# Performance work log

Measured on AMD Instinct MI355X. Metric: run time of the kernel, lower is better.

Reference implementation:

```python
import jax, jax.numpy as jnp
import numpy as np

NEG_BIG = -9e15

def setup_inputs() -> dict:
    key = jax.random.key(0)
    k1, k2, k3, k4 = jax.random.split(key, 4)
    N, Fin, Fout = 8192, 256, 128
    x = jax.random.normal(k1, (N, Fin), dtype=jnp.float32)
    adj = jax.random.randint(k2, (N, N), 0, 2, dtype=jnp.int32)
    # xavier-uniform-like init
    limW = float(np.sqrt(6.0 / (Fin + Fout)))
    W = jax.random.uniform(k3, (Fin, Fout), minval=-limW, maxval=limW, dtype=jnp.float32)
    lima = float(np.sqrt(6.0 / (2 * Fout + 1)))
    a = jax.random.uniform(k4, (2 * Fout, 1), minval=-lima, maxval=lima, dtype=jnp.float32)
    return {"x": x, "adj": adj, "W": W, "a": a}

def reference(x, adj, W, a, alpha=0.2):
    # h: (N, Fout)
    h = x @ W
    Fout = W.shape[1]
    # Split a into source/target halves: e[i,j] = leakyrelu(h_i·a1 + h_j·a2)
    a1, a2 = a[:Fout, 0], a[Fout:, 0]
    s = h @ a1  # (N,) row (source) scores
    t = h @ a2  # (N,) col (target) scores
    e = jax.nn.leaky_relu(s[:, None] + t[None, :], negative_slope=alpha)  # (N, N)
    e = jnp.where(adj > 0, e, NEG_BIG)
    attention = jax.nn.softmax(e, axis=1)
    # dropout omitted (eval mode / training=False)
    return attention @ h
```

## Files before the change

kernel.cpp:

```cpp
#include <hip/hip_runtime.h>
#include <hip/hip_bf16.h>

typedef __attribute__((ext_vector_type(8))) short short8;
typedef __attribute__((ext_vector_type(4))) short short4v;
typedef __attribute__((ext_vector_type(4))) float f32x4;

#define NR 8192
#define LOG2E 1.4426950408889634f

__device__ __forceinline__ short f2bf(float f) {
  return __builtin_bit_cast(short, __float2bfloat16(f));
}

__global__ __launch_bounds__(256) void k_gemm_h(const float* __restrict__ x,
                                                const float* __restrict__ W,
                                                const float* __restrict__ a,
                                                short* __restrict__ HT2,
                                                float* __restrict__ sv,
                                                float* __restrict__ tv) {
  __shared__ short WT[128][136];
  const int tid = threadIdx.x;
  const int w = tid >> 6;
  const int L = tid & 63;
  const int lm = L & 15;
  const int q = L >> 4;
  const int i0 = blockIdx.x * 64;

  f32x4 acc[8];
#pragma unroll
  for (int nn = 0; nn < 8; ++nn) acc[nn] = (f32x4){0.f, 0.f, 0.f, 0.f};

  for (int kc = 0; kc < 256; kc += 128) {
    if (kc) __syncthreads();
#pragma unroll
    for (int p = 0; p < 16; ++p) {
      int idx = p * 256 + tid;
      int k = idx >> 5;
      int f4 = (idx & 31) * 4;
      float4 v = *(const float4*)&W[(kc + k) * 128 + f4];
      WT[f4 + 0][k] = f2bf(v.x);
      WT[f4 + 1][k] = f2bf(v.y);
      WT[f4 + 2][k] = f2bf(v.z);
      WT[f4 + 3][k] = f2bf(v.w);
    }
    __syncthreads();
#pragma unroll
    for (int ks = 0; ks < 4; ++ks) {
      int row = i0 + 16 * w + lm;
      const float* xp = &x[(size_t)row * 256 + kc + ks * 32 + q * 8];
      float4 xa = *(const float4*)xp;
      float4 xb = *(const float4*)(xp + 4);
      short8 af;
      af[0] = f2bf(xa.x); af[1] = f2bf(xa.y); af[2] = f2bf(xa.z); af[3] = f2bf(xa.w);
      af[4] = f2bf(xb.x); af[5] = f2bf(xb.y); af[6] = f2bf(xb.z); af[7] = f2bf(xb.w);
#pragma unroll
      for (int nn = 0; nn < 8; ++nn) {
        short8 bf = *(const short8*)&WT[nn * 16 + lm][ks * 32 + q * 8];
        acc[nn] = __builtin_amdgcn_mfma_f32_16x16x32_bf16(af, bf, acc[nn], 0, 0, 0);
      }
    }
  }

  const int ib = i0 + 16 * w + 4 * q;
  const int tbase = (ib >> 5) * 4096 + (ib & 31);
  float a1v[8], a2v[8];
#pragma unroll
  for (int nn = 0; nn < 8; ++nn) {
    a1v[nn] = a[nn * 16 + lm];
    a2v[nn] = a[128 + nn * 16 + lm];
  }
  float sr[4] = {0.f, 0.f, 0.f, 0.f};
  float tr[4] = {0.f, 0.f, 0.f, 0.f};
#pragma unroll
  for (int nn = 0; nn < 8; ++nn) {
    int f = nn * 16 + lm;
    short4v o;
    o[0] = f2bf(acc[nn][0]);
    o[1] = f2bf(acc[nn][1]);
    o[2] = f2bf(acc[nn][2]);
    o[3] = f2bf(acc[nn][3]);
    *(short4v*)&HT2[tbase + f * 32] = o;
#pragma unroll
    for (int r = 0; r < 4; ++r) {
      sr[r] += acc[nn][r] * a1v[nn];
      tr[r] += acc[nn][r] * a2v[nn];
    }
  }
#pragma unroll
  for (int d = 1; d < 16; d <<= 1) {
#pragma unroll
    for (int r = 0; r < 4; ++r) {
      sr[r] += __shfl_xor(sr[r], d);
      tr[r] += __shfl_xor(tr[r], d);
    }
  }
  if (lm == 0) {
#pragma unroll
    for (int r = 0; r < 4; ++r) {
      sv[ib + r] = sr[r] * LOG2E;
      tv[ib + r] = tr[r] * LOG2E;
    }
  }
}

__global__ __launch_bounds__(256, 2) void k_flash(const int* __restrict__ adj,
                                                  const short* __restrict__ HT2,
                                                  const float* __restrict__ sv,
                                                  const float* __restrict__ tv,
                                                  float* __restrict__ part,
                                                  float* __restrict__ lpart) {
  __shared__ short lds_s[32768];
  unsigned* ldsw = (unsigned*)lds_s;
  const int tid = threadIdx.x;
  const int w = tid >> 6;
  const int L = tid & 63;
  const int lm = L & 15;
  const int q = L >> 4;
  const int sp = blockIdx.x & 15;
  const int it = blockIdx.x >> 4;
  const int i0 = it * 128;

  const int row0 = i0 + 32 * w + lm;
  const int row1 = row0 + 16;
  const float s0 = sv[row0];
  const float s1 = sv[row1];
  const size_t ar0 = (size_t)row0 * NR;
  const size_t ar1 = (size_t)row1 * NR;

  f32x4 acc[2][8];
#pragma unroll
  for (int mm = 0; mm < 2; ++mm)
#pragma unroll
    for (int nn = 0; nn < 8; ++nn) acc[mm][nn] = (f32x4){0.f, 0.f, 0.f, 0.f};
  float l0 = 0.f, l1 = 0.f;

  const int tile0 = sp * 16;
  int jb = tile0 * 32 + q * 8;
  int4 sa00 = *(const int4*)&adj[ar0 + jb];
  int4 sa01 = *(const int4*)&adj[ar0 + jb + 4];
  int4 sa10 = *(const int4*)&adj[ar1 + jb];
  int4 sa11 = *(const int4*)&adj[ar1 + jb + 4];

  for (int t = 0; t < 16; ++t) {
    if ((t & 7) == 0) {
      __syncthreads();
      const int pbase_t = tile0 + t;
#pragma unroll
      for (int z = 0; z < 16; ++z) {
        int id = z * 256 + tid;
        int tt = id >> 9;
        int k = id & 511;
        int f = k >> 2, c = k & 3;
        uint4 v = *(const uint4*)&HT2[(size_t)(pbase_t + tt) * 4096 + k * 8];
        int cs = c ^ ((f >> 1) & 3);
        *(uint4*)&ldsw[tt * 2048 + f * 16 + cs * 4] = v;
      }
      __syncthreads();
    }
    int4 a00 = sa00, a01 = sa01, a10 = sa10, a11 = sa11;
    if (t + 1 < 16) {
      int jn = (tile0 + t + 1) * 32 + q * 8;
      sa00 = *(const int4*)&adj[ar0 + jn];
      sa01 = *(const int4*)&adj[ar0 + jn + 4];
      sa10 = *(const int4*)&adj[ar1 + jn];
      sa11 = *(const int4*)&adj[ar1 + jn + 4];
    }
    const int jc = (tile0 + t) * 32 + q * 8;
    float4 tv0 = *(const float4*)&tv[jc];
    float4 tv1 = *(const float4*)&tv[jc + 4];
    const int tt = t & 7;
    short8 bf[8];
#pragma unroll
    for (int nn = 0; nn < 8; ++nn) {
      int f = nn * 16 + lm;
      bf[nn] = *(const short8*)&ldsw[tt * 2048 + f * 16 + ((q ^ ((f >> 1) & 3)) * 4)];
    }

    int av0[8] = {a00.x, a00.y, a00.z, a00.w, a01.x, a01.y, a01.z, a01.w};
    int av1[8] = {a10.x, a10.y, a10.z, a10.w, a11.x, a11.y, a11.z, a11.w};
    float tvl[8] = {tv0.x, tv0.y, tv0.z, tv0.w, tv1.x, tv1.y, tv1.z, tv1.w};
    short8 p0, p1;
#pragma unroll
    for (int e = 0; e < 8; ++e) {
      float v0 = s0 + tvl[e];
      float e0 = fmaxf(v0, 0.2f * v0);
      float pp0 = (av0[e] > 0) ? __builtin_amdgcn_exp2f(e0) : 0.f;
      l0 += pp0;
      p0[e] = f2bf(pp0);
      float v1 = s1 + tvl[e];
      float e1 = fmaxf(v1, 0.2f * v1);
      float pp1 = (av1[e] > 0) ? __builtin_amdgcn_exp2f(e1) : 0.f;
      l1 += pp1;
      p1[e] = f2bf(pp1);
    }
#pragma unroll
    for (int nn = 0; nn < 8; ++nn) {
      acc[0][nn] = __builtin_amdgcn_mfma_f32_16x16x32_bf16(p0, bf[nn], acc[0][nn], 0, 0, 0);
      acc[1][nn] = __builtin_amdgcn_mfma_f32_16x16x32_bf16(p1, bf[nn], acc[1][nn], 0, 0, 0);
    }
  }
  __syncthreads();

  float* my = (float*)lds_s + w * 2048;
#pragma unroll
  for (int mm = 0; mm < 2; ++mm) {
#pragma unroll
    for (int nn = 0; nn < 8; ++nn)
#pragma unroll
      for (int r = 0; r < 4; ++r)
        my[(4 * q + r) * 128 + nn * 16 + lm] = acc[mm][nn][r];
    float* pbase = part + ((size_t)sp * NR + i0 + 32 * w + 16 * mm) * 128;
#pragma unroll
    for (int c = 0; c < 8; ++c) {
      int idx = (c * 64 + L) * 4;
      *(float4*)&pbase[idx] = *(const float4*)&my[idx];
    }
  }

  l0 += __shfl_xor(l0, 16);
  l0 += __shfl_xor(l0, 32);
  l1 += __shfl_xor(l1, 16);
  l1 += __shfl_xor(l1, 32);
  if (q == 0) {
    lpart[sp * NR + row0] = l0;
    lpart[sp * NR + row1] = l1;
  }
}

__global__ __launch_bounds__(256) void k_reduce(const float* __restrict__ part,
                                                const float* __restrict__ lpart,
                                                float* __restrict__ out, int S) {
  int idx4 = blockIdx.x * 256 + threadIdx.x;
  int idx = idx4 * 4;
  int i = idx >> 7;
  float4 sum = {0.f, 0.f, 0.f, 0.f};
  for (int sp = 0; sp < S; ++sp) {
    float4 v = *(const float4*)&part[(size_t)sp * (NR * 128) + idx];
    sum.x += v.x; sum.y += v.y; sum.z += v.z; sum.w += v.w;
  }
  float l = 0.f;
  for (int sp = 0; sp < S; ++sp) l += lpart[sp * NR + i];
  float inv = (l > 0.f) ? 1.f / l : 0.f;
  float4 o = {sum.x * inv, sum.y * inv, sum.z * inv, sum.w * inv};
  *(float4*)&out[idx] = o;
}

extern "C" void kernel_launch(void* const* d_in, const int* in_sizes, int n_in,
                              void* d_out, int out_size, void* d_ws, size_t ws_size,
                              hipStream_t stream) {
  const float* x = (const float*)d_in[0];
  const int* adj = (const int*)d_in[1];
  const float* W = (const float*)d_in[2];
  const float* a = (const float*)d_in[3];
  float* out = (float*)d_out;

  char* ws = (char*)d_ws;
  short* HT2 = (short*)(ws + 0);
  float* sv = (float*)(ws + 2097152);
  float* tv = (float*)(ws + 2129920);
  float* lpart = (float*)(ws + 2162688);
  float* part = (float*)(ws + 2719744);

  const int S = 16;

  hipLaunchKernelGGL(k_gemm_h, dim3(128), dim3(256), 0, stream, x, W, a, HT2, sv, tv);
  hipLaunchKernelGGL(k_flash, dim3(64 * S), dim3(256), 0, stream, adj, HT2, sv, tv,
                     part, lpart);
  hipLaunchKernelGGL(k_reduce, dim3((NR * 128) / 1024), dim3(256), 0, stream, part,
                     lpart, out, S);
}
```

Measured before the change: 423.6 us.

## Split flash block into 8 waves with one 16-row MFMA tile each

The attention kernel now launches 512-thread blocks where each of the 8 waves owns one 16-row strip instead of two. This halves per-wave accumulators and adj prefetch registers and raises launch bounds to 4 blocks per CU, aiming at higher occupancy to hide the latency of the adjacency stream. In exchange, each B fragment read from LDS now feeds one MFMA per wave instead of two, so LDS read traffic per FLOP doubles. Staging of HT2 into LDS is also spread across twice as many threads.

```diff
diff --git a/kernel.cpp b/kernel.cpp
--- a/kernel.cpp
+++ b/kernel.cpp
@@ -103,7 +103,7 @@
   }
 }
 
-__global__ __launch_bounds__(256, 2) void k_flash(const int* __restrict__ adj,
+__global__ __launch_bounds__(512, 4) void k_flash(const int* __restrict__ adj,
                                                   const short* __restrict__ HT2,
                                                   const float* __restrict__ sv,
                                                   const float* __restrict__ tv,
@@ -120,34 +120,27 @@
   const int it = blockIdx.x >> 4;
   const int i0 = it * 128;
 
-  const int row0 = i0 + 32 * w + lm;
-  const int row1 = row0 + 16;
+  const int row0 = i0 + 16 * w + lm;
   const float s0 = sv[row0];
-  const float s1 = sv[row1];
   const size_t ar0 = (size_t)row0 * NR;
-  const size_t ar1 = (size_t)row1 * NR;
-
-  f32x4 acc[2][8];
-#pragma unroll
-  for (int mm = 0; mm < 2; ++mm)
-#pragma unroll
-    for (int nn = 0; nn < 8; ++nn) acc[mm][nn] = (f32x4){0.f, 0.f, 0.f, 0.f};
-  float l0 = 0.f, l1 = 0.f;
+
+  f32x4 acc[8];
+#pragma unroll
+  for (int nn = 0; nn < 8; ++nn) acc[nn] = (f32x4){0.f, 0.f, 0.f, 0.f};
+  float l0 = 0.f;
 
   const int tile0 = sp * 16;
   int jb = tile0 * 32 + q * 8;
   int4 sa00 = *(const int4*)&adj[ar0 + jb];
   int4 sa01 = *(const int4*)&adj[ar0 + jb + 4];
-  int4 sa10 = *(const int4*)&adj[ar1 + jb];
-  int4 sa11 = *(const int4*)&adj[ar1 + jb + 4];
 
   for (int t = 0; t < 16; ++t) {
     if ((t & 7) == 0) {
       __syncthreads();
       const int pbase_t = tile0 + t;
 #pragma unroll
-      for (int z = 0; z < 16; ++z) {
-        int id = z * 256 + tid;
+      for (int z = 0; z < 8; ++z) {
+        int id = z * 512 + tid;
         int tt = id >> 9;
         int k = id & 511;
         int f = k >> 2, c = k & 3;
@@ -157,13 +150,11 @@
       }
       __syncthreads();
     }
-    int4 a00 = sa00, a01 = sa01, a10 = sa10, a11 = sa11;
+    int4 a00 = sa00, a01 = sa01;
     if (t + 1 < 16) {
       int jn = (tile0 + t + 1) * 32 + q * 8;
       sa00 = *(const int4*)&adj[ar0 + jn];
       sa01 = *(const int4*)&adj[ar0 + jn + 4];
-      sa10 = *(const int4*)&adj[ar1 + jn];
-      sa11 = *(const int4*)&adj[ar1 + jn + 4];
     }
     const int jc = (tile0 + t) * 32 + q * 8;
     float4 tv0 = *(const float4*)&tv[jc];
@@ -177,9 +168,8 @@
     }
 
     int av0[8] = {a00.x, a00.y, a00.z, a00.w, a01.x, a01.y, a01.z, a01.w};
-    int av1[8] = {a10.x, a10.y, a10.z, a10.w, a11.x, a11.y, a11.z, a11.w};
     float tvl[8] = {tv0.x, tv0.y, tv0.z, tv0.w, tv1.x, tv1.y, tv1.z, tv1.w};
-    short8 p0, p1;
+    short8 p0;
 #pragma unroll
     for (int e = 0; e < 8; ++e) {
       float v0 = s0 + tvl[e];
@@ -187,44 +177,29 @@
       float pp0 = (av0[e] > 0) ? __builtin_amdgcn_exp2f(e0) : 0.f;
       l0 += pp0;
       p0[e] = f2bf(pp0);
-      float v1 = s1 + tvl[e];
-      float e1 = fmaxf(v1, 0.2f * v1);
-      float pp1 = (av1[e] > 0) ? __builtin_amdgcn_exp2f(e1) : 0.f;
-      l1 += pp1;
-      p1[e] = f2bf(pp1);
-    }
-#pragma unroll
-    for (int nn = 0; nn < 8; ++nn) {
-      acc[0][nn] = __builtin_amdgcn_mfma_f32_16x16x32_bf16(p0, bf[nn], acc[0][nn], 0, 0, 0);
-      acc[1][nn] = __builtin_amdgcn_mfma_f32_16x16x32_bf16(p1, bf[nn], acc[1][nn], 0, 0, 0);
-    }
+    }
+#pragma unroll
+    for (int nn = 0; nn < 8; ++nn)
+      acc[nn] = __builtin_amdgcn_mfma_f32_16x16x32_bf16(p0, bf[nn], acc[nn], 0, 0, 0);
   }
   __syncthreads();
 
   float* my = (float*)lds_s + w * 2048;
 #pragma unroll
-  for (int mm = 0; mm < 2; ++mm) {
-#pragma unroll
-    for (int nn = 0; nn < 8; ++nn)
-#pragma unroll
-      for (int r = 0; r < 4; ++r)
-        my[(4 * q + r) * 128 + nn * 16 + lm] = acc[mm][nn][r];
-    float* pbase = part + ((size_t)sp * NR + i0 + 32 * w + 16 * mm) * 128;
-#pragma unroll
-    for (int c = 0; c < 8; ++c) {
-      int idx = (c * 64 + L) * 4;
-      *(float4*)&pbase[idx] = *(const float4*)&my[idx];
-    }
+  for (int nn = 0; nn < 8; ++nn)
+#pragma unroll
+    for (int r = 0; r < 4; ++r)
+      my[(4 * q + r) * 128 + nn * 16 + lm] = acc[nn][r];
+  float* pbase = part + ((size_t)sp * NR + i0 + 16 * w) * 128;
+#pragma unroll
+  for (int c = 0; c < 8; ++c) {
+    int idx = (c * 64 + L) * 4;
+    *(float4*)&pbase[idx] = *(const float4*)&my[idx];
   }
 
   l0 += __shfl_xor(l0, 16);
   l0 += __shfl_xor(l0, 32);
-  l1 += __shfl_xor(l1, 16);
-  l1 += __shfl_xor(l1, 32);
-  if (q == 0) {
-    lpart[sp * NR + row0] = l0;
-    lpart[sp * NR + row1] = l1;
-  }
+  if (q == 0) lpart[sp * NR + row0] = l0;
 }
 
 __global__ __launch_bounds__(256) void k_reduce(const float* __restrict__ part,
@@ -264,7 +239,7 @@
   const int S = 16;
 
   hipLaunchKernelGGL(k_gemm_h, dim3(128), dim3(256), 0, stream, x, W, a, HT2, sv, tv);
-  hipLaunchKernelGGL(k_flash, dim3(64 * S), dim3(256), 0, stream, adj, HT2, sv, tv,
+  hipLaunchKernelGGL(k_flash, dim3(64 * S), dim3(512), 0, stream, adj, HT2, sv, tv,
                      part, lpart);
   hipLaunchKernelGGL(k_reduce, dim3((NR * 128) / 1024), dim3(256), 0, stream, part,
                      lpart, out, S);
```

After: 415.8 us. Within noise of the previous version (-1.8%).
